# Optimization experiments

Measured on AMD Instinct MI355X. Metric: run time of the kernel, lower is better.

Reference implementation:

```python
import jax, jax.numpy as jnp
import numpy as np

D_MODEL, D_STATE, D_CONV, EXPAND = 768, 16, 4, 2
D_INNER = EXPAND * D_MODEL
DT_RANK = -(-D_MODEL // 16)  # ceil(d_model/16) = 48
LN_EPS = 1e-5


def setup_inputs() -> dict:
    key = jax.random.key(0)
    ks = jax.random.split(key, 12)
    B, L = 8, 1024
    s = 0.02
    x = jax.random.normal(ks[0], (B, L, D_MODEL), jnp.float32)
    ln_g = jnp.ones((D_MODEL,), jnp.float32)
    ln_b = jnp.zeros((D_MODEL,), jnp.float32)
    W_in = jax.random.normal(ks[1], (D_MODEL, 2 * D_INNER), jnp.float32) * s
    conv_w = jax.random.normal(ks[2], (D_INNER, 1, D_CONV), jnp.float32) * s
    conv_b = jnp.zeros((D_INNER,), jnp.float32)
    W_x = jax.random.normal(ks[3], (D_INNER, DT_RANK + 2 * D_STATE), jnp.float32) * s
    W_dt = jax.random.normal(ks[4], (DT_RANK, D_INNER), jnp.float32) * s
    b_dt = jax.random.uniform(ks[5], (D_INNER,), jnp.float32, -4.0, -2.0)  # softplus -> small dt
    # S4D-real init: A_log[d, n] = log(n+1)
    A_log = jnp.log(jnp.tile(jnp.arange(1, D_STATE + 1, dtype=jnp.float32), (D_INNER, 1)))
    Dskip = jnp.ones((D_INNER,), jnp.float32)
    W_out = jax.random.normal(ks[6], (D_INNER, D_MODEL), jnp.float32) * s
    return dict(x=x, ln_g=ln_g, ln_b=ln_b, W_in=W_in, conv_w=conv_w, conv_b=conv_b,
                W_x=W_x, W_dt=W_dt, b_dt=b_dt, A_log=A_log, Dskip=Dskip, W_out=W_out)


def _mamba_mixer(x, ln_g, ln_b, W_in, conv_w, conv_b, W_x, W_dt, b_dt, A_log, Dskip, W_out):
    B, L, _ = x.shape
    d_inner, _, d_conv = conv_w.shape
    d_state = A_log.shape[1]

    # LayerNorm
    mu = x.mean(-1, keepdims=True)
    var = ((x - mu) ** 2).mean(-1, keepdims=True)
    xn = (x - mu) * jax.lax.rsqrt(var + LN_EPS) * ln_g + ln_b

    # Input projection -> (x_part, z gate)
    xz = xn @ W_in                      # (B, L, 2*d_inner)
    xp, z = jnp.split(xz, 2, axis=-1)

    # Causal depthwise conv1d over time
    xc = jax.lax.conv_general_dilated(
        xp.transpose(0, 2, 1), conv_w,
        window_strides=(1,), padding=[(d_conv - 1, 0)],
        dimension_numbers=("NCH", "OIH", "NCH"), feature_group_count=d_inner)
    xc = jax.nn.silu(xc + conv_b[None, :, None]).transpose(0, 2, 1)  # (B, L, d_inner)

    # Selective parameters
    x_dbl = xc @ W_x                    # (B, L, dt_rank + 2*d_state)
    dt, Bm, Cm = jnp.split(x_dbl, [DT_RANK, DT_RANK + d_state], axis=-1)
    dt = jax.nn.softplus(dt @ W_dt + b_dt)   # (B, L, d_inner)
    A = -jnp.exp(A_log)                      # (d_inner, d_state)

    # Selective (S6) scan over time, carrying state h: (B, d_inner, d_state)
    def step(h, inp):
        x_t, dt_t, B_t, C_t = inp            # (B,d_in), (B,d_in), (B,d_state), (B,d_state)
        dA = jnp.exp(dt_t[:, :, None] * A)   # (B, d_inner, d_state)
        h = dA * h + dt_t[:, :, None] * B_t[:, None, :] * x_t[:, :, None]
        y = jnp.einsum('bds,bs->bd', h, C_t)
        return h, y

    h0 = jnp.zeros((B, d_inner, d_state), x.dtype)
    xs = (xc.transpose(1, 0, 2), dt.transpose(1, 0, 2),
          Bm.transpose(1, 0, 2), Cm.transpose(1, 0, 2))
    _, ys = jax.lax.scan(step, h0, xs)       # ys: (L, B, d_inner)
    y = ys.transpose(1, 0, 2) + xc * Dskip

    # Gate, output projection, residual (dropout is identity in eval mode)
    y = y * jax.nn.silu(z)
    return y @ W_out + x


def reference(x, ln_g, ln_b, W_in, conv_w, conv_b, W_x, W_dt, b_dt, A_log, Dskip, W_out):
    return _mamba_mixer(x, ln_g, ln_b, W_in, conv_w, conv_b, W_x, W_dt, b_dt, A_log, Dskip, W_out)
```

## Files before the change

### kernel.cpp

```cpp
#include <hip/hip_runtime.h>

typedef unsigned short u16;
typedef unsigned int u32;
typedef u16 u16x4 __attribute__((ext_vector_type(4)));
typedef u16 u16x8 __attribute__((ext_vector_type(8)));
typedef __bf16 bf16x8 __attribute__((ext_vector_type(8)));
typedef float f32x4 __attribute__((ext_vector_type(4)));

#define DEV static __device__ __forceinline__

DEV float bf2f(u16 u) {
  union { u32 i; float f; } c; c.i = ((u32)u) << 16; return c.f;
}
DEV u16 f2bf(float f) {
  union { float f; u32 i; } c; c.f = f;
  u32 x = c.i;
  return (u16)((x + 0x7fffu + ((x >> 16) & 1u)) >> 16);
}

__global__ __launch_bounds__(256) void k_ln(const float* __restrict__ x, const float* __restrict__ g,
                                            const float* __restrict__ b, u16* __restrict__ xn) {
  int row = blockIdx.x, t = threadIdx.x;
  const float* xr = x + (size_t)row * 768;
  float v0 = xr[t], v1 = xr[t + 256], v2 = xr[t + 512];
  float s = v0 + v1 + v2, s2 = v0 * v0 + v1 * v1 + v2 * v2;
#pragma unroll
  for (int o = 32; o; o >>= 1) { s += __shfl_xor(s, o, 64); s2 += __shfl_xor(s2, o, 64); }
  __shared__ float ps[4], ps2[4];
  int wv = t >> 6;
  if ((t & 63) == 0) { ps[wv] = s; ps2[wv] = s2; }
  __syncthreads();
  s = ps[0] + ps[1] + ps[2] + ps[3];
  s2 = ps2[0] + ps2[1] + ps2[2] + ps2[3];
  float mu = s * (1.f / 768.f);
  float var = s2 * (1.f / 768.f) - mu * mu;
  float rs = rsqrtf(var + 1e-5f);
  u16* o = xn + (size_t)row * 768;
  o[t]       = f2bf((v0 - mu) * rs * g[t]       + b[t]);
  o[t + 256] = f2bf((v1 - mu) * rs * g[t + 256] + b[t + 256]);
  o[t + 512] = f2bf((v2 - mu) * rs * g[t + 512] + b[t + 512]);
}

__global__ __launch_bounds__(256) void k_prep(const float* __restrict__ Win, const float* __restrict__ Wout,
                                              const float* __restrict__ Wx,
                                              u16* __restrict__ Wt_in, u16* __restrict__ Wt_out,
                                              u16* __restrict__ Wxt) {
  int bid = blockIdx.x, tid = threadIdx.x;
  if (bid < 3456) {
    const float* in; u16* out; int R, C, bx, by;
    if (bid < 2304) { in = Win;  out = Wt_in;  R = 768;  C = 3072; bx = bid % 96; by = bid / 96; }
    else { int b2 = bid - 2304; in = Wout; out = Wt_out; R = 1536; C = 768;  bx = b2 % 24; by = b2 / 24; }
    __shared__ u16 tile[32][33];
    int tx = tid & 31, ty = tid >> 5;
    int x = bx * 32 + tx, y0 = by * 32;
#pragma unroll
    for (int j = 0; j < 32; j += 8)
      tile[ty + j][tx] = f2bf(in[(size_t)(y0 + ty + j) * C + x]);
    __syncthreads();
    int ox = y0 + tx, oy0 = bx * 32;
#pragma unroll
    for (int j = 0; j < 32; j += 8)
      out[(size_t)(oy0 + ty + j) * R + ox] = tile[tx][ty + j];
  } else {
    int idx = (bid - 3456) * 256 + tid;
    int c = idx / 1536, r = idx % 1536;
    Wxt[idx] = (c < 80) ? f2bf(Wx[(size_t)r * 80 + c]) : (u16)0;
  }
}

__global__ __launch_bounds__(256) void k_wdt_prep(const float* __restrict__ Wdt, u16* __restrict__ Wdtt) {
  int idx = blockIdx.x * 256 + threadIdx.x;
  int n = idx >> 6, k = idx & 63;
  Wdtt[idx] = (k < 48) ? f2bf(Wdt[(size_t)k * 1536 + n]) : (u16)0;
}

template <bool OUTF32, int ACT, int TM, bool SPLITK>
__global__ __launch_bounds__(256) void k_gemm(const u16* __restrict__ A, const u16* __restrict__ Bt,
                                              void* __restrict__ Cout, void* __restrict__ C2,
                                              const float* __restrict__ resid, int N, int K, int splitN,
                                              int lda, int ldb, const float* __restrict__ bias) {
  __shared__ u16 As[TM * 64];
  __shared__ u16 Bs[128 * 64];
  constexpr int MI = TM / 32;
  int tid = threadIdx.x;
  int wave = tid >> 6, lane = tid & 63;
  int l15 = lane & 15, l4 = lane >> 4;
  int m0 = blockIdx.y * TM, n0 = blockIdx.x * 128;
  int wm = (wave >> 1) * (TM / 2), wn = (wave & 1) * 64;
  int rs = tid >> 3, ss = tid & 7;
  int kOff = SPLITK ? blockIdx.z * K : 0;
  const u16* gA = A  + (size_t)(m0 + rs) * lda + kOff + (size_t)(ss ^ (rs & 7)) * 8;
  const u16* gB = Bt + (size_t)(n0 + rs) * ldb + kOff + (size_t)(ss ^ (rs & 7)) * 8;
  char* ldsA = (char*)As + wave * 1024;
  char* ldsB = (char*)Bs + wave * 1024;
  const u16* aAddr[MI][2];
  const u16* bAddr[4][2];
#pragma unroll
  for (int i = 0; i < MI; ++i) {
    int row = wm + i * 16 + l15;
#pragma unroll
    for (int h = 0; h < 2; ++h)
      aAddr[i][h] = As + row * 64 + ((h * 4 + l4) ^ (row & 7)) * 8;
  }
#pragma unroll
  for (int j = 0; j < 4; ++j) {
    int row = wn + j * 16 + l15;
#pragma unroll
    for (int h = 0; h < 2; ++h)
      bAddr[j][h] = Bs + row * 64 + ((h * 4 + l4) ^ (row & 7)) * 8;
  }
  f32x4 acc[MI][4] = {};
  for (int k0 = 0; k0 < K; k0 += 64) {
    __syncthreads();
#pragma unroll
    for (int j = 0; j < MI; ++j)
      __builtin_amdgcn_global_load_lds(
          (const __attribute__((address_space(1))) void*)(gA + k0 + (size_t)j * 32 * lda),
          (__attribute__((address_space(3))) void*)(ldsA + j * 4096), 16, 0, 0);
#pragma unroll
    for (int j = 0; j < 4; ++j)
      __builtin_amdgcn_global_load_lds(
          (const __attribute__((address_space(1))) void*)(gB + k0 + (size_t)j * 32 * ldb),
          (__attribute__((address_space(3))) void*)(ldsB + j * 4096), 16, 0, 0);
    __syncthreads();
    union FragU { u16x8 q; bf16x8 v; } af[MI][2], bfr[4][2];
#pragma unroll
    for (int i = 0; i < MI; ++i) {
      af[i][0].q = *(const u16x8*)aAddr[i][0];
      af[i][1].q = *(const u16x8*)aAddr[i][1];
    }
#pragma unroll
    for (int j = 0; j < 4; ++j) {
      bfr[j][0].q = *(const u16x8*)bAddr[j][0];
      bfr[j][1].q = *(const u16x8*)bAddr[j][1];
    }
#pragma unroll
    for (int h = 0; h < 2; ++h)
#pragma unroll
      for (int i = 0; i < MI; ++i)
#pragma unroll
        for (int j = 0; j < 4; ++j)
          acc[i][j] = __builtin_amdgcn_mfma_f32_16x16x32_bf16(af[i][h].v, bfr[j][h].v, acc[i][j], 0, 0, 0);
  }
  bool hi = n0 >= splitN;
  int strideOut = hi ? (N - splitN) : splitN;
  int nBase = (hi ? (n0 - splitN) : n0) + wn;
  void* base = hi ? C2 : Cout;
  size_t partOff = SPLITK ? (size_t)blockIdx.z * (size_t)(gridDim.y * TM) * (size_t)strideOut : 0;
#pragma unroll
  for (int i = 0; i < MI; ++i) {
#pragma unroll
    for (int r = 0; r < 4; ++r) {
      int row = m0 + wm + i * 16 + l4 * 4 + r;
      const float* rrow = resid ? (resid + (size_t)row * strideOut + nBase) : nullptr;
#pragma unroll
      for (int j = 0; j < 4; ++j) {
        float v = acc[i][j][r];
        int col = j * 16 + l15;
        if (rrow) v += rrow[col];
        if (ACT == 1) {
          v += bias[nBase + col];
          v = (v > 20.f) ? v : __logf(1.f + __expf(v));
        }
        if (OUTF32)
          ((float*)base)[partOff + (size_t)row * strideOut + nBase + col] = v;
        else
          ((u16*)base)[(size_t)row * strideOut + nBase + col] = f2bf(v);
      }
    }
  }
}

__global__ __launch_bounds__(256) void k_xd_red(const float* __restrict__ part, u16* __restrict__ xd) {
  int i = (blockIdx.x * 256 + threadIdx.x) * 4;
  f32x4 s = *(const f32x4*)(part + i);
#pragma unroll
  for (int q = 1; q < 4; ++q) {
    f32x4 p = *(const f32x4*)(part + (size_t)q * 1048576 + i);
    s[0] += p[0]; s[1] += p[1]; s[2] += p[2]; s[3] += p[3];
  }
  u16x4 o = { f2bf(s[0]), f2bf(s[1]), f2bf(s[2]), f2bf(s[3]) };
  *(u16x4*)(xd + i) = o;
}

__global__ __launch_bounds__(256) void k_conv(const u16* __restrict__ xp, const float* __restrict__ cw,
                                              const float* __restrict__ cb, u16* __restrict__ xc) {
  int idx = blockIdx.x * 256 + threadIdx.x;
  int d8 = idx % 192;
  int blq = idx / 192;
  int lq = blq & 255;
  int b = blq >> 8;
  int l0 = lq * 4;
  int d0 = d8 * 8;

  f32x4 w[8];
#pragma unroll
  for (int e = 0; e < 8; ++e) w[e] = *(const f32x4*)(cw + (d0 + e) * 4);
  f32x4 bi0 = *(const f32x4*)(cb + d0);
  f32x4 bi1 = *(const f32x4*)(cb + d0 + 4);

  const u16* xb = xp + ((size_t)b * 1024) * 1536 + d0;
  u16x8 xrow[7];
#pragma unroll
  for (int j = 0; j < 7; ++j) {
    int l = l0 - 3 + j;
    if (l >= 0) xrow[j] = *(const u16x8*)(xb + (size_t)l * 1536);
    else { u16x8 zz = {}; xrow[j] = zz; }
  }

  u16* ob = xc + ((size_t)b * 1024 + l0) * 1536 + d0;
#pragma unroll
  for (int t = 0; t < 4; ++t) {
    u16x8 o;
#pragma unroll
    for (int e = 0; e < 8; ++e) {
      float acc = (e < 4) ? bi0[e] : bi1[e - 4];
#pragma unroll
      for (int j = 0; j < 4; ++j)
        acc = fmaf(bf2f(xrow[t + j][e]), w[e][j], acc);
      o[e] = f2bf(acc / (1.f + __expf(-acc)));
    }
    *(u16x8*)(ob + (size_t)t * 1536) = o;
  }
}

__global__ __launch_bounds__(256) void k_scanA(const u16* __restrict__ dt, const u16* __restrict__ xc,
                                               const u16* __restrict__ xd, const float* __restrict__ Alog,
                                               float* __restrict__ hp, float* __restrict__ Pp) {
  int d = blockIdx.x * 256 + threadIdx.x;
  int c = blockIdx.y, b = blockIdx.z;
  float An[16];
#pragma unroll
  for (int n = 0; n < 16; ++n) An[n] = -__expf(Alog[d * 16 + n]);
  float h[16] = {};
  float sdt = 0.f;
  size_t t0 = (size_t)b * 1024 + c * 64;
  const u16* dtp = dt + t0 * 1536 + d;
  const u16* xcp = xc + t0 * 1536 + d;
  const u16* xdp = xd + t0 * 128;
  for (int l = 0; l < 64; ++l) {
    float dtv = bf2f(dtp[(size_t)l * 1536]);
    float xv  = bf2f(xcp[(size_t)l * 1536]);
    u16x8 b0 = *(const u16x8*)(xdp + l * 128 + 48);
    u16x8 b1 = *(const u16x8*)(xdp + l * 128 + 56);
    float dx = dtv * xv;
    sdt += dtv;
#pragma unroll
    for (int n = 0; n < 16; ++n) {
      float dA = __expf(dtv * An[n]);
      float Bv = bf2f(n < 8 ? b0[n] : b1[n - 8]);
      h[n] = fmaf(dA, h[n], dx * Bv);
    }
  }
  size_t s = (((size_t)(b * 16 + c) * 1536) + d) * 16;
#pragma unroll
  for (int q = 0; q < 4; ++q) {
    f32x4 hv = { h[q * 4], h[q * 4 + 1], h[q * 4 + 2], h[q * 4 + 3] };
    f32x4 pv = { __expf(An[q * 4] * sdt), __expf(An[q * 4 + 1] * sdt),
                 __expf(An[q * 4 + 2] * sdt), __expf(An[q * 4 + 3] * sdt) };
    *(f32x4*)(hp + s + q * 4) = hv;
    *(f32x4*)(Pp + s + q * 4) = pv;
  }
}

__global__ __launch_bounds__(256) void k_scanB(float* __restrict__ hp, const float* __restrict__ Pp) {
  int dn = blockIdx.x * 256 + threadIdx.x;
  int b = blockIdx.y;
  float h = 0.f;
#pragma unroll
  for (int c = 0; c < 16; ++c) {
    size_t s = ((size_t)(b * 16 + c)) * 24576 + dn;
    float p = Pp[s], v = hp[s];
    hp[s] = h;
    h = fmaf(p, h, v);
  }
}

__global__ __launch_bounds__(256) void k_scanC(u16* xcY, const u16* __restrict__ dt,
                                               const u16* __restrict__ xd, const u16* __restrict__ z,
                                               const float* __restrict__ Alog, const float* __restrict__ Dsk,
                                               const float* __restrict__ hp) {
  int d = blockIdx.x * 256 + threadIdx.x;
  int c = blockIdx.y, b = blockIdx.z;
  float An[16];
#pragma unroll
  for (int n = 0; n < 16; ++n) An[n] = -__expf(Alog[d * 16 + n]);
  float h[16];
  size_t s = (((size_t)(b * 16 + c) * 1536) + d) * 16;
#pragma unroll
  for (int q = 0; q < 4; ++q) {
    f32x4 hv = *(const f32x4*)(hp + s + q * 4);
    h[q * 4] = hv[0]; h[q * 4 + 1] = hv[1]; h[q * 4 + 2] = hv[2]; h[q * 4 + 3] = hv[3];
  }
  float Dv = Dsk[d];
  size_t t0 = (size_t)b * 1024 + c * 64;
  const u16* dtp = dt + t0 * 1536 + d;
  u16* xcp = xcY + t0 * 1536 + d;
  const u16* zp = z + t0 * 1536 + d;
  const u16* xdp = xd + t0 * 128;
  for (int l = 0; l < 64; ++l) {
    float dtv = bf2f(dtp[(size_t)l * 1536]);
    float xv  = bf2f(xcp[(size_t)l * 1536]);
    float zv  = bf2f(zp[(size_t)l * 1536]);
    u16x8 b0 = *(const u16x8*)(xdp + l * 128 + 48);
    u16x8 b1 = *(const u16x8*)(xdp + l * 128 + 56);
    u16x8 c0 = *(const u16x8*)(xdp + l * 128 + 64);
    u16x8 c1 = *(const u16x8*)(xdp + l * 128 + 72);
    float dx = dtv * xv;
    float y0 = 0.f, y1 = 0.f, y2 = 0.f, y3 = 0.f;
#pragma unroll
    for (int n = 0; n < 16; ++n) {
      float dA = __expf(dtv * An[n]);
      float Bv = bf2f(n < 8 ? b0[n] : b1[n - 8]);
      float Cv = bf2f(n < 8 ? c0[n] : c1[n - 8]);
      h[n] = fmaf(dA, h[n], dx * Bv);
      float hc = h[n] * Cv;
      if ((n & 3) == 0) y0 += hc; else if ((n & 3) == 1) y1 += hc;
      else if ((n & 3) == 2) y2 += hc; else y3 += hc;
    }
    float y = (y0 + y1) + (y2 + y3);
    float gate = zv / (1.f + __expf(-zv));
    xcp[(size_t)l * 1536] = f2bf((y + xv * Dv) * gate);
  }
}

extern "C" void kernel_launch(void* const* d_in, const int* in_sizes, int n_in,
                              void* d_out, int out_size, void* d_ws, size_t ws_size,
                              hipStream_t stream) {
  const float* x      = (const float*)d_in[0];
  const float* ln_g   = (const float*)d_in[1];
  const float* ln_b   = (const float*)d_in[2];
  const float* W_in   = (const float*)d_in[3];
  const float* conv_w = (const float*)d_in[4];
  const float* conv_b = (const float*)d_in[5];
  const float* W_x    = (const float*)d_in[6];
  const float* W_dt   = (const float*)d_in[7];
  const float* b_dt   = (const float*)d_in[8];
  const float* A_log  = (const float*)d_in[9];
  const float* Dskip  = (const float*)d_in[10];
  const float* W_out  = (const float*)d_in[11];

  char* ws = (char*)d_ws;
  u16* xn     = (u16*)(ws);
  float* hp   = (float*)(ws);
  u16* Wt_in  = (u16*)(ws + 12582912);
  u16* Wdtt   = (u16*)(ws + 12582912);
  u16* Wt_out = (u16*)(ws + 17301504);
  u16* Wxt    = (u16*)(ws + 19660800);
  u16* xp     = (u16*)(ws + 20054016);
  float* Pp   = (float*)(ws + 20054016);
  u16* z      = (u16*)(ws + 45219840);
  u16* xc     = (u16*)(ws + 70385664);
  u16* xd     = (u16*)(ws + 95551488);
  u16* dt     = (u16*)(ws + 97648640);
  float* xdP  = (float*)(ws + 97648640);

  k_prep<<<4224, 256, 0, stream>>>(W_in, W_out, W_x, Wt_in, Wt_out, Wxt);
  k_ln<<<8192, 256, 0, stream>>>(x, ln_g, ln_b, xn);
  k_gemm<false, 0, 128, false><<<dim3(24, 64), 256, 0, stream>>>(xn, Wt_in, xp, z, nullptr, 3072, 768, 1536, 768, 768, nullptr);
  k_conv<<<1536, 256, 0, stream>>>(xp, conv_w, conv_b, xc);
  k_wdt_prep<<<384, 256, 0, stream>>>(W_dt, Wdtt);
  k_gemm<true, 0, 64, true><<<dim3(1, 128, 4), 256, 0, stream>>>(xc, Wxt, xdP, nullptr, nullptr, 128, 384, 128, 1536, 1536, nullptr);
  k_xd_red<<<1024, 256, 0, stream>>>(xdP, xd);
  k_gemm<false, 1, 128, false><<<dim3(12, 64), 256, 0, stream>>>(xd, Wdtt, dt, nullptr, nullptr, 1536, 64, 1536, 128, 64, b_dt);
  k_scanA<<<dim3(6, 16, 8), 256, 0, stream>>>(dt, xc, xd, A_log, hp, Pp);
  k_scanB<<<dim3(96, 8), 256, 0, stream>>>(hp, Pp);
  k_scanC<<<dim3(6, 16, 8), 256, 0, stream>>>(xc, dt, xd, z, A_log, Dskip, hp);
  k_gemm<true, 0, 64, false><<<dim3(6, 128), 256, 0, stream>>>(xc, Wt_out, d_out, nullptr, x, 768, 1536, 768, 1536, 1536, nullptr);
}
```

Baseline: 275.9 us.

## Double-buffer GEMM LDS tiles to overlap global loads with MFMA

Converts the GEMM K-loop to a two-stage LDS double buffer. The next tile is issued with global_load_lds before computing the current one, and a partial vmcnt wait lets the loads overlap the MFMAs. It also raises wave priority around the MFMA block. LDS use doubles, which may lower occupancy. The hand-counted vmcnt values must match the number of outstanding loads for each TM.

```diff
diff --git a/kernel.cpp b/kernel.cpp
--- a/kernel.cpp
+++ b/kernel.cpp
@@ -8,6 +8,8 @@
 typedef float f32x4 __attribute__((ext_vector_type(4)));
 
 #define DEV static __device__ __forceinline__
+#define AS1 __attribute__((address_space(1)))
+#define AS3 __attribute__((address_space(3)))
 
 DEV float bf2f(u16 u) {
   union { u32 i; float f; } c; c.i = ((u32)u) << 16; return c.f;
@@ -79,8 +81,8 @@
                                               void* __restrict__ Cout, void* __restrict__ C2,
                                               const float* __restrict__ resid, int N, int K, int splitN,
                                               int lda, int ldb, const float* __restrict__ bias) {
-  __shared__ u16 As[TM * 64];
-  __shared__ u16 Bs[128 * 64];
+  __shared__ u16 As[2][TM * 64];
+  __shared__ u16 Bs[2][128 * 64];
   constexpr int MI = TM / 32;
   int tid = threadIdx.x;
   int wave = tid >> 6, lane = tid & 63;
@@ -91,49 +93,61 @@
   int kOff = SPLITK ? blockIdx.z * K : 0;
   const u16* gA = A  + (size_t)(m0 + rs) * lda + kOff + (size_t)(ss ^ (rs & 7)) * 8;
   const u16* gB = Bt + (size_t)(n0 + rs) * ldb + kOff + (size_t)(ss ^ (rs & 7)) * 8;
-  char* ldsA = (char*)As + wave * 1024;
-  char* ldsB = (char*)Bs + wave * 1024;
-  const u16* aAddr[MI][2];
-  const u16* bAddr[4][2];
+  int aOff[MI][2], bOff[4][2];
 #pragma unroll
   for (int i = 0; i < MI; ++i) {
     int row = wm + i * 16 + l15;
 #pragma unroll
-    for (int h = 0; h < 2; ++h)
-      aAddr[i][h] = As + row * 64 + ((h * 4 + l4) ^ (row & 7)) * 8;
+    for (int h = 0; h < 2; ++h) aOff[i][h] = row * 64 + ((h * 4 + l4) ^ (row & 7)) * 8;
   }
 #pragma unroll
   for (int j = 0; j < 4; ++j) {
     int row = wn + j * 16 + l15;
 #pragma unroll
-    for (int h = 0; h < 2; ++h)
-      bAddr[j][h] = Bs + row * 64 + ((h * 4 + l4) ^ (row & 7)) * 8;
-  }
+    for (int h = 0; h < 2; ++h) bOff[j][h] = row * 64 + ((h * 4 + l4) ^ (row & 7)) * 8;
+  }
+  auto stage = [&](int kt, int buf) {
+    char* dA = (char*)(&As[buf][0]) + wave * 1024;
+    char* dB = (char*)(&Bs[buf][0]) + wave * 1024;
+    int k0 = kt * 64;
+#pragma unroll
+    for (int j = 0; j < MI; ++j)
+      __builtin_amdgcn_global_load_lds((const AS1 void*)(gA + k0 + (size_t)j * 32 * lda),
+                                       (AS3 void*)(dA + j * 4096), 16, 0, 0);
+#pragma unroll
+    for (int j = 0; j < 4; ++j)
+      __builtin_amdgcn_global_load_lds((const AS1 void*)(gB + k0 + (size_t)j * 32 * ldb),
+                                       (AS3 void*)(dB + j * 4096), 16, 0, 0);
+  };
   f32x4 acc[MI][4] = {};
-  for (int k0 = 0; k0 < K; k0 += 64) {
-    __syncthreads();
-#pragma unroll
-    for (int j = 0; j < MI; ++j)
-      __builtin_amdgcn_global_load_lds(
-          (const __attribute__((address_space(1))) void*)(gA + k0 + (size_t)j * 32 * lda),
-          (__attribute__((address_space(3))) void*)(ldsA + j * 4096), 16, 0, 0);
-#pragma unroll
-    for (int j = 0; j < 4; ++j)
-      __builtin_amdgcn_global_load_lds(
-          (const __attribute__((address_space(1))) void*)(gB + k0 + (size_t)j * 32 * ldb),
-          (__attribute__((address_space(3))) void*)(ldsB + j * 4096), 16, 0, 0);
-    __syncthreads();
+  int nt = K >> 6;
+  stage(0, 0);
+  int cur = 0;
+  for (int t = 0; t < nt; ++t) {
+    if (t + 1 < nt) stage(t + 1, cur ^ 1);
+    __builtin_amdgcn_sched_barrier(0);
+    if (t + 1 < nt) {
+      if constexpr (TM == 128) asm volatile("s_waitcnt vmcnt(8)" ::: "memory");
+      else                     asm volatile("s_waitcnt vmcnt(6)" ::: "memory");
+    } else {
+      asm volatile("s_waitcnt vmcnt(0)" ::: "memory");
+    }
+    __builtin_amdgcn_s_barrier();
+    __builtin_amdgcn_sched_barrier(0);
+    const u16* ab = &As[cur][0];
+    const u16* bb = &Bs[cur][0];
     union FragU { u16x8 q; bf16x8 v; } af[MI][2], bfr[4][2];
 #pragma unroll
     for (int i = 0; i < MI; ++i) {
-      af[i][0].q = *(const u16x8*)aAddr[i][0];
-      af[i][1].q = *(const u16x8*)aAddr[i][1];
+      af[i][0].q = *(const u16x8*)(ab + aOff[i][0]);
+      af[i][1].q = *(const u16x8*)(ab + aOff[i][1]);
     }
 #pragma unroll
     for (int j = 0; j < 4; ++j) {
-      bfr[j][0].q = *(const u16x8*)bAddr[j][0];
-      bfr[j][1].q = *(const u16x8*)bAddr[j][1];
-    }
+      bfr[j][0].q = *(const u16x8*)(bb + bOff[j][0]);
+      bfr[j][1].q = *(const u16x8*)(bb + bOff[j][1]);
+    }
+    __builtin_amdgcn_s_setprio(1);
 #pragma unroll
     for (int h = 0; h < 2; ++h)
 #pragma unroll
@@ -141,6 +155,10 @@
 #pragma unroll
         for (int j = 0; j < 4; ++j)
           acc[i][j] = __builtin_amdgcn_mfma_f32_16x16x32_bf16(af[i][h].v, bfr[j][h].v, acc[i][j], 0, 0, 0);
+    __builtin_amdgcn_s_setprio(0);
+    __builtin_amdgcn_sched_barrier(0);
+    __builtin_amdgcn_s_barrier();
+    cur ^= 1;
   }
   bool hi = n0 >= splitN;
   int strideOut = hi ? (N - splitN) : splitN;
```

Result: faster. 267.8 us (-2.9%).
